# Kernel tuning notes

Hardware: AMD Instinct MI355X
Metric: run time of the kernel (lower is better)

The kernel has to match this reference:

```python
import jax, jax.numpy as jnp
import numpy as np

EMBED_DIM = 1024
NUM_HEADS = 16
HEAD_DIM = EMBED_DIM // NUM_HEADS


def setup_inputs() -> dict:
    key = jax.random.key(0)
    ks = jax.random.split(key, 5)
    B, T, C = 2, 2048, EMBED_DIM
    s_in = 1.0 / np.sqrt(C)
    x = jax.random.normal(ks[0], (B, T, C), dtype=jnp.float32)
    W_qkv = jax.random.normal(ks[1], (C, 3 * C), dtype=jnp.float32) * s_in
    b_qkv = jnp.zeros((3 * C,), dtype=jnp.float32)
    W_out = jax.random.normal(ks[2], (C, C), dtype=jnp.float32) * s_in
    b_out = jnp.zeros((C,), dtype=jnp.float32)
    return {"x": x, "W_qkv": W_qkv, "b_qkv": b_qkv, "W_out": W_out, "b_out": b_out}


def reference(x, W_qkv, b_qkv, W_out, b_out):
    B, T, C = x.shape
    H, D = NUM_HEADS, HEAD_DIM
    qkv = x @ W_qkv + b_qkv                      # [B,T,3C]
    qkv = qkv.reshape(B, T, 3, H, D)
    q = jnp.transpose(qkv[:, :, 0], (0, 2, 1, 3))  # [B,H,T,D]
    k = jnp.transpose(qkv[:, :, 1], (0, 2, 1, 3))
    v = jnp.transpose(qkv[:, :, 2], (0, 2, 1, 3))
    scores = jnp.einsum('bhtd,bhsd->bhts', q, k) / np.sqrt(D).astype(jnp.float32)
    attn = jax.nn.softmax(scores, axis=-1)
    ctx = jnp.einsum('bhts,bhsd->bhtd', attn, v)   # [B,H,T,D]
    ctx = jnp.transpose(ctx, (0, 2, 1, 3)).reshape(B, T, C)
    return ctx @ W_out + b_out
```

## Files before the change

kernel.cpp:

```cpp
#include <hip/hip_runtime.h>
#include <hip/hip_bf16.h>


typedef __attribute__((ext_vector_type(8)))  short short8;
typedef __attribute__((ext_vector_type(4)))  float floatx4;
typedef __attribute__((ext_vector_type(16))) float floatx16;

__device__ inline ushort f2bf(float f) {
    union { __hip_bfloat16 h; ushort u; } c; c.h = __float2bfloat16(f); return c.u;
}

__device__ inline uint cvt_pk_bf16(float a, float b) {
    uint r;
    asm("v_cvt_pk_bf16_f32 %0, %1, %2" : "=v"(r) : "v"(a), "v"(b));
    return r;
}

__device__ inline void gld16(const ushort* g, ushort* l) {
    __builtin_amdgcn_global_load_lds(
        (__attribute__((address_space(1))) void*)(g),
        (__attribute__((address_space(3))) void*)(l), 16, 0, 0);
}

__device__ inline void tile_transpose(const float* __restrict__ src, ushort* __restrict__ dst,
                                      int R, int C, int rt, int ct, int t, ushort* L)
{
    const int row = t >> 2, cc = (t & 3) * 16;
    const float* sp = src + (long)(rt * 64 + row) * C + ct * 64 + cc;
    ushort tmp[16];
    #pragma unroll
    for (int i = 0; i < 4; i++) {
        float4 v = *(const float4*)(sp + i * 4);
        tmp[i*4+0]=f2bf(v.x); tmp[i*4+1]=f2bf(v.y); tmp[i*4+2]=f2bf(v.z); tmp[i*4+3]=f2bf(v.w);
    }
    *(uint4*)&L[row * 72 + cc]     = *(uint4*)&tmp[0];
    *(uint4*)&L[row * 72 + cc + 8] = *(uint4*)&tmp[8];
    __syncthreads();
    const int c = t >> 2, rc = (t & 3) * 16;
    ushort o[16];
    #pragma unroll
    for (int j = 0; j < 16; j++) o[j] = L[(rc + j) * 72 + c];
    ushort* dp = dst + (long)(ct * 64 + c) * R + rt * 64 + rc;
    *(uint4*)dp       = *(uint4*)&o[0];
    *(uint4*)(dp + 8) = *(uint4*)&o[8];
}

__global__ __launch_bounds__(256) void prep_kernel(
    const float* __restrict__ x, const float* __restrict__ Wqkv, const float* __restrict__ Wout,
    ushort* __restrict__ xb, ushort* __restrict__ wqkvT, ushort* __restrict__ woutT)
{
    __shared__ __align__(16) ushort L[64 * 72];
    const int bid = blockIdx.x, t = threadIdx.x;
    if (bid < 2048) {
        long i = ((long)bid * 256 + t) * 8;
        float4 a = *(const float4*)(x + i);
        float4 b = *(const float4*)(x + i + 4);
        ushort tmp[8] = { f2bf(a.x), f2bf(a.y), f2bf(a.z), f2bf(a.w),
                          f2bf(b.x), f2bf(b.y), f2bf(b.z), f2bf(b.w) };
        *(uint4*)(xb + i) = *(uint4*)tmp;
    } else if (bid < 2048 + 768) {
        int idx = bid - 2048;
        tile_transpose(Wqkv, wqkvT, 1024, 3072, idx & 15, idx >> 4, t, L);
    } else {
        int idx = bid - 2048 - 768;
        tile_transpose(Wout, woutT, 1024, 1024, idx & 15, idx >> 4, t, L);
    }
}

#define QSCALE 0.18033688011112042f

__global__ __launch_bounds__(256, 3) void qkv_gemm_kernel(
    const ushort* __restrict__ A, const ushort* __restrict__ Bt,
    const float* __restrict__ bias,
    ushort* __restrict__ qbuf, ushort* __restrict__ kbuf, ushort* __restrict__ vtG)
{
    __shared__ __align__(16) ushort SMEM[16384];

    const int t = threadIdx.x;
    const int w = t >> 6, lane = t & 63;
    const int r = lane & 15, qq = lane >> 4;
    const int wm = w >> 1, wn = w & 1;

    const int id = blockIdx.x;
    const int xcd = id & 7, cidx = id >> 3;
    const int lx = cidx % 12, ly = cidx / 12;
    const int bx = (xcd & 1) * 12 + lx;
    const int by = (xcd >> 1) * 8 + ly;
    const int rowBase = by * 128, colBase = bx * 128;

    const int s_row = lane >> 2, s_k = (lane & 3) * 8;
    const ushort* aS = A  + (long)(rowBase + w * 32 + s_row) * 1024 + s_k;
    const ushort* bS = Bt + (long)(colBase + w * 32 + s_row) * 1024 + s_k;

    floatx4 acc[4][4] = {};

    gld16(aS,             SMEM + w * 1024);
    gld16(aS + 16 * 1024, SMEM + w * 1024 + 512);
    gld16(bS,             SMEM + 4096 + w * 1024);
    gld16(bS + 16 * 1024, SMEM + 4096 + w * 1024 + 512);
    __syncthreads();

    #pragma unroll 2
    for (int k = 0; k < 32; k++) {
        ushort* cur = SMEM + (k & 1) * 8192;
        if (k < 31) {
            ushort* nxt = SMEM + ((k + 1) & 1) * 8192;
            const int ko = (k + 1) * 32;
            gld16(aS + ko,             nxt + w * 1024);
            gld16(aS + ko + 16 * 1024, nxt + w * 1024 + 512);
            gld16(bS + ko,             nxt + 4096 + w * 1024);
            gld16(bS + ko + 16 * 1024, nxt + 4096 + w * 1024 + 512);
        }
        short8 af[4], bf4[4];
        #pragma unroll
        for (int tm = 0; tm < 4; tm++) af[tm]  = *(const short8*)&cur[(wm * 64 + tm * 16 + r) * 32 + qq * 8];
        #pragma unroll
        for (int tn = 0; tn < 4; tn++) bf4[tn] = *(const short8*)&cur[4096 + (wn * 64 + tn * 16 + r) * 32 + qq * 8];
        #pragma unroll
        for (int tm = 0; tm < 4; tm++)
            #pragma unroll
            for (int tn = 0; tn < 4; tn++)
                acc[tm][tn] = __builtin_amdgcn_mfma_f32_16x16x32_bf16(af[tm], bf4[tn], acc[tm][tn], 0, 0, 0);
        __syncthreads();
    }

    if (colBase < 2048) {
        #pragma unroll
        for (int tn = 0; tn < 4; tn++) {
            int col = colBase + wn * 64 + tn * 16 + r;
            float bvv = bias[col];
            #pragma unroll
            for (int tm = 0; tm < 4; tm++) {
                #pragma unroll
                for (int reg = 0; reg < 4; reg++) {
                    int row = rowBase + wm * 64 + tm * 16 + qq * 4 + reg;
                    float val = acc[tm][tn][reg] + bvv;
                    if (colBase < 1024) qbuf[(long)row * 1024 + col]        = f2bf(val * QSCALE);
                    else                kbuf[(long)row * 1024 + col - 1024] = f2bf(val);
                }
            }
        }
    } else {
        ushort* L = SMEM;
        #pragma unroll
        for (int hh = 0; hh < 2; hh++) {
            __syncthreads();
            if (wn == hh) {
                #pragma unroll
                for (int tn = 0; tn < 4; tn++) {
                    int vc = tn * 16 + r;
                    float bvv = bias[colBase + wn * 64 + vc];
                    #pragma unroll
                    for (int tm = 0; tm < 4; tm++) {
                        int row0 = wm * 64 + tm * 16 + qq * 4;
                        ushort q4[4] = { f2bf(acc[tm][tn][0] + bvv), f2bf(acc[tm][tn][1] + bvv),
                                         f2bf(acc[tm][tn][2] + bvv), f2bf(acc[tm][tn][3] + bvv) };
                        *(uint2*)&L[vc * 136 + row0] = *(uint2*)q4;
                    }
                }
            }
            __syncthreads();
            int d = t >> 2, tq = (t & 3) * 32;
            int h_loc = ((colBase - 2048) >> 6) + hh;
            long vtrow = (long)((rowBase >> 11) * 16 + h_loc) * 64 + d;
            ushort* dst = vtG + vtrow * 2048 + (rowBase & 2047) + tq;
            #pragma unroll
            for (int i = 0; i < 4; i++)
                *(uint4*)(dst + 8 * i) = *(uint4*)&L[d * 136 + tq + 8 * i];
        }
    }
}

__global__ __launch_bounds__(256) void out_gemm_kernel(
    const ushort* __restrict__ A, const ushort* __restrict__ Bt,
    const float* __restrict__ bias, float* __restrict__ out)
{
    __shared__ __align__(16) ushort SMEM[12288];

    const int t = threadIdx.x;
    const int w = t >> 6, lane = t & 63;
    const int r = lane & 15, qq = lane >> 4;
    const int wm = w >> 1, wn = w & 1;

    const int id = blockIdx.x;
    const int xcd = id & 7, cidx = id >> 3;
    const int bx = (xcd & 1) * 8 + (cidx & 7);
    const int by = (xcd >> 1) * 8 + (cidx >> 3);
    const int rowBase = by * 128, colBase = bx * 64;

    const int s_row = lane >> 2, s_k = (lane & 3) * 8;
    const ushort* aS = A  + (long)(rowBase + w * 32 + s_row) * 1024 + s_k;
    const ushort* bS = Bt + (long)(colBase + w * 16 + s_row) * 1024 + s_k;

    floatx4 acc[4][2] = {};

    gld16(aS,             SMEM + w * 1024);
    gld16(aS + 16 * 1024, SMEM + w * 1024 + 512);
    gld16(bS,             SMEM + 4096 + w * 512);
    __syncthreads();

    #pragma unroll 2
    for (int k = 0; k < 32; k++) {
        ushort* cur = SMEM + (k & 1) * 6144;
        if (k < 31) {
            ushort* nxt = SMEM + ((k + 1) & 1) * 6144;
            const int ko = (k + 1) * 32;
            gld16(aS + ko,             nxt + w * 1024);
            gld16(aS + ko + 16 * 1024, nxt + w * 1024 + 512);
            gld16(bS + ko,             nxt + 4096 + w * 512);
        }
        short8 af[4], bf2[2];
        #pragma unroll
        for (int tm = 0; tm < 4; tm++) af[tm]  = *(const short8*)&cur[(wm * 64 + tm * 16 + r) * 32 + qq * 8];
        #pragma unroll
        for (int tn = 0; tn < 2; tn++) bf2[tn] = *(const short8*)&cur[4096 + (wn * 32 + tn * 16 + r) * 32 + qq * 8];
        #pragma unroll
        for (int tm = 0; tm < 4; tm++)
            #pragma unroll
            for (int tn = 0; tn < 2; tn++)
                acc[tm][tn] = __builtin_amdgcn_mfma_f32_16x16x32_bf16(af[tm], bf2[tn], acc[tm][tn], 0, 0, 0);
        __syncthreads();
    }

    #pragma unroll
    for (int tn = 0; tn < 2; tn++) {
        int col = colBase + wn * 32 + tn * 16 + r;
        float bvv = bias[col];
        #pragma unroll
        for (int tm = 0; tm < 4; tm++) {
            #pragma unroll
            for (int reg = 0; reg < 4; reg++) {
                int row = rowBase + wm * 64 + tm * 16 + qq * 4 + reg;
                out[(long)row * 1024 + col] = acc[tm][tn][reg] + bvv;
            }
        }
    }
}

__global__ __launch_bounds__(512, 4) void attn_kernel(
    ushort* __restrict__ qbuf, const ushort* __restrict__ kbuf,
    const ushort* __restrict__ vt)
{
    __shared__ __align__(16) ushort SM[2][2][2][64 * 72];

    const int t = threadIdx.x;
    const int w = t >> 6, lane = t & 63;
    const int m32 = lane & 31, hi = lane >> 5;
    const int h2 = w >> 2, wq = w & 3;

    const int id = blockIdx.x;
    const int j = id >> 3;
    const int bh = (id & 7) * 4 + (j >> 4);
    const int qt = j & 15;
    const int b = bh >> 4, h = bh & 15;
    const long qrow = (long)(b * 2048 + qt * 128 + wq * 32 + m32);

    short8 qfrag[4];
    #pragma unroll
    for (int dc = 0; dc < 4; dc++)
        qfrag[dc] = *(const short8*)(qbuf + qrow * 1024 + h * 64 + dc * 16 + hi * 8);

    short8 vones;
    #pragma unroll
    for (int i = 0; i < 8; i++) vones[i] = (short)0x3F80;

    const int ts = t & 255;
    const int srow = ts >> 2, scol = (ts & 3) * 16;
    const ushort* kP = kbuf + (long)(b * 2048 + h2 * 1024 + srow) * 1024 + h * 64 + scol;
    const ushort* vP = vt + (long)(bh * 64 + srow) * 2048 + h2 * 1024 + scol;

    floatx16 o[2] = {};
    floatx16 lacc = {};

    uint4 kr0, kr1, vr0, vr1;

    kr0 = *(const uint4*)kP;  kr1 = *(const uint4*)(kP + 8);
    vr0 = *(const uint4*)vP;  vr1 = *(const uint4*)(vP + 8);
    {
        ushort* Ks = SM[h2][0][0]; ushort* Vs = SM[h2][0][1];
        *(uint4*)&Ks[srow * 72 + scol]     = kr0;
        *(uint4*)&Ks[srow * 72 + scol + 8] = kr1;
        *(uint4*)&Vs[srow * 72 + scol]     = vr0;
        *(uint4*)&Vs[srow * 72 + scol + 8] = vr1;
    }
    kr0 = *(const uint4*)(kP + 64 * 1024); kr1 = *(const uint4*)(kP + 64 * 1024 + 8);
    vr0 = *(const uint4*)(vP + 64);        vr1 = *(const uint4*)(vP + 64 + 8);
    __syncthreads();

    #pragma unroll 2
    for (int tt = 0; tt < 16; tt++) {
        ushort* Ks = SM[h2][tt & 1][0];
        ushort* Vs = SM[h2][tt & 1][1];

        floatx16 s[2] = {};
        __builtin_amdgcn_s_setprio(1);
        #pragma unroll
        for (int c = 0; c < 2; c++) {
            #pragma unroll
            for (int dc = 0; dc < 4; dc++) {
                short8 kf = *(const short8*)&Ks[(c * 32 + m32) * 72 + dc * 16 + hi * 8];
                s[c] = __builtin_amdgcn_mfma_f32_32x32x16_bf16(kf, qfrag[dc], s[c], 0, 0, 0);
            }
        }
        __builtin_amdgcn_s_setprio(0);

        if (tt < 15) {
            ushort* Kn = SM[h2][(tt + 1) & 1][0];
            ushort* Vn = SM[h2][(tt + 1) & 1][1];
            *(uint4*)&Kn[srow * 72 + scol]     = kr0;
            *(uint4*)&Kn[srow * 72 + scol + 8] = kr1;
            *(uint4*)&Vn[srow * 72 + scol]     = vr0;
            *(uint4*)&Vn[srow * 72 + scol + 8] = vr1;
            if (tt < 14) {
                const ushort* kp = kP + (long)(tt + 2) * 64 * 1024;
                const ushort* vp = vP + (tt + 2) * 64;
                kr0 = *(const uint4*)kp; kr1 = *(const uint4*)(kp + 8);
                vr0 = *(const uint4*)vp; vr1 = *(const uint4*)(vp + 8);
            }
        }

        uint pk[2][8];
        #pragma unroll
        for (int c = 0; c < 2; c++) {
            #pragma unroll
            for (int i = 0; i < 8; i++) {
                float p0 = __builtin_amdgcn_exp2f(s[c][2 * i]);
                float p1 = __builtin_amdgcn_exp2f(s[c][2 * i + 1]);
                pk[c][i] = cvt_pk_bf16(p0, p1);
            }
        }

        __builtin_amdgcn_s_setprio(1);
        #pragma unroll
        for (int c = 0; c < 2; c++) {
            #pragma unroll
            for (int kc = 0; kc < 2; kc++) {
                uint a0 = pk[c][4 * kc + 0], b0 = pk[c][4 * kc + 2];
                asm("v_permlane32_swap_b32 %0, %1" : "+v"(a0), "+v"(b0));
                uint a1 = pk[c][4 * kc + 1], b1 = pk[c][4 * kc + 3];
                asm("v_permlane32_swap_b32 %0, %1" : "+v"(a1), "+v"(b1));
                union { uint u[4]; short8 s8; } cv;
                cv.u[0] = a0; cv.u[1] = a1; cv.u[2] = b0; cv.u[3] = b1;
                #pragma unroll
                for (int dt = 0; dt < 2; dt++) {
                    short8 vf = *(const short8*)&Vs[(dt * 32 + m32) * 72 + c * 32 + kc * 16 + hi * 8];
                    o[dt] = __builtin_amdgcn_mfma_f32_32x32x16_bf16(vf, cv.s8, o[dt], 0, 0, 0);
                }
                lacc = __builtin_amdgcn_mfma_f32_32x32x16_bf16(vones, cv.s8, lacc, 0, 0, 0);
            }
        }
        __builtin_amdgcn_s_setprio(0);

        __syncthreads();
    }

    float* OL = (float*)SM;
    float* LL = OL + 4 * 2048;
    if (h2 == 1) {
        #pragma unroll
        for (int dt = 0; dt < 2; dt++)
            #pragma unroll
            for (int i = 0; i < 16; i++)
                OL[wq * 2048 + (dt * 16 + i) * 64 + lane] = o[dt][i];
        LL[wq * 64 + lane] = lacc[0];
    }
    __syncthreads();
    if (h2 == 0) {
        float inv = 1.f / (lacc[0] + LL[wq * 64 + lane]);
        #pragma unroll
        for (int dt = 0; dt < 2; dt++) {
            #pragma unroll
            for (int i = 0; i < 16; i++) o[dt][i] += OL[wq * 2048 + (dt * 16 + i) * 64 + lane];
            #pragma unroll
            for (int g = 0; g < 4; g++) {
                ushort tmp[4] = { f2bf(o[dt][4*g+0] * inv), f2bf(o[dt][4*g+1] * inv),
                                  f2bf(o[dt][4*g+2] * inv), f2bf(o[dt][4*g+3] * inv) };
                *(uint2*)(qbuf + qrow * 1024 + h * 64 + dt * 32 + g * 8 + hi * 4) = *(uint2*)tmp;
            }
        }
    }
}

extern "C" void kernel_launch(void* const* d_in, const int* in_sizes, int n_in,
                              void* d_out, int out_size, void* d_ws, size_t ws_size,
                              hipStream_t stream) {
    const float* x     = (const float*)d_in[0];
    const float* W_qkv = (const float*)d_in[1];
    const float* b_qkv = (const float*)d_in[2];
    const float* W_out = (const float*)d_in[3];
    const float* b_out = (const float*)d_in[4];
    float* out = (float*)d_out;

    ushort* qbuf  = (ushort*)d_ws;
    ushort* kbuf  = qbuf + (size_t)4096 * 1024;
    ushort* vt    = kbuf + (size_t)4096 * 1024;
    ushort* woutT = vt + (size_t)2048 * 2048;
    ushort* wqkvT = woutT + (size_t)1024 * 1024;

    ushort* xb    = (ushort*)d_out;

    dim3 blk(256);
    prep_kernel<<<3072, blk, 0, stream>>>(x, W_qkv, W_out, xb, wqkvT, woutT);
    qkv_gemm_kernel<<<768, blk, 0, stream>>>(xb, wqkvT, b_qkv, qbuf, kbuf, vt);
    attn_kernel<<<512, dim3(512), 0, stream>>>(qbuf, kbuf, vt);
    out_gemm_kernel<<<512, blk, 0, stream>>>(qbuf, woutT, b_out, out);
}
```

Baseline: 187.2 us.

## Drop KV split in attention; each block handles 256 queries over full KV

Before, each block had two wave groups that each covered half the key/value sequence for 128 queries, and their partial outputs were merged through shared memory. Now all 8 waves work on 256 different query rows, sharing one K/V tile stream over the whole sequence, and the grid is halved. This removes the cross-group merge and doubles K/V tile reuse per block. The costs are a serial loop twice as long per block, only 256 blocks (about one per CU), and a lower launch-bounds occupancy hint, which may leave less latency hiding.

```diff
diff --git a/kernel.cpp b/kernel.cpp
--- a/kernel.cpp
+++ b/kernel.cpp
@@ -237,23 +237,22 @@
     }
 }
 
-__global__ __launch_bounds__(512, 4) void attn_kernel(
+__global__ __launch_bounds__(512, 2) void attn_kernel(
     ushort* __restrict__ qbuf, const ushort* __restrict__ kbuf,
     const ushort* __restrict__ vt)
 {
-    __shared__ __align__(16) ushort SM[2][2][2][64 * 72];
+    __shared__ __align__(16) ushort SM[2][2][64 * 72];
 
     const int t = threadIdx.x;
     const int w = t >> 6, lane = t & 63;
     const int m32 = lane & 31, hi = lane >> 5;
-    const int h2 = w >> 2, wq = w & 3;
 
     const int id = blockIdx.x;
     const int j = id >> 3;
-    const int bh = (id & 7) * 4 + (j >> 4);
-    const int qt = j & 15;
+    const int bh = (id & 7) * 4 + (j >> 3);
+    const int qt = j & 7;
     const int b = bh >> 4, h = bh & 15;
-    const long qrow = (long)(b * 2048 + qt * 128 + wq * 32 + m32);
+    const long qrow = (long)(b * 2048 + qt * 256 + w * 32 + m32);
 
     short8 qfrag[4];
     #pragma unroll
@@ -264,33 +263,27 @@
     #pragma unroll
     for (int i = 0; i < 8; i++) vones[i] = (short)0x3F80;
 
-    const int ts = t & 255;
-    const int srow = ts >> 2, scol = (ts & 3) * 16;
-    const ushort* kP = kbuf + (long)(b * 2048 + h2 * 1024 + srow) * 1024 + h * 64 + scol;
-    const ushort* vP = vt + (long)(bh * 64 + srow) * 2048 + h2 * 1024 + scol;
+    const int srow = t >> 3, scol = (t & 7) * 8;
+    const ushort* kP = kbuf + (long)(b * 2048 + srow) * 1024 + h * 64 + scol;
+    const ushort* vP = vt + (long)(bh * 64 + srow) * 2048 + scol;
 
     floatx16 o[2] = {};
     floatx16 lacc = {};
 
-    uint4 kr0, kr1, vr0, vr1;
-
-    kr0 = *(const uint4*)kP;  kr1 = *(const uint4*)(kP + 8);
-    vr0 = *(const uint4*)vP;  vr1 = *(const uint4*)(vP + 8);
-    {
-        ushort* Ks = SM[h2][0][0]; ushort* Vs = SM[h2][0][1];
-        *(uint4*)&Ks[srow * 72 + scol]     = kr0;
-        *(uint4*)&Ks[srow * 72 + scol + 8] = kr1;
-        *(uint4*)&Vs[srow * 72 + scol]     = vr0;
-        *(uint4*)&Vs[srow * 72 + scol + 8] = vr1;
-    }
-    kr0 = *(const uint4*)(kP + 64 * 1024); kr1 = *(const uint4*)(kP + 64 * 1024 + 8);
-    vr0 = *(const uint4*)(vP + 64);        vr1 = *(const uint4*)(vP + 64 + 8);
+    uint4 kr0, vr0;
+
+    kr0 = *(const uint4*)kP;
+    vr0 = *(const uint4*)vP;
+    *(uint4*)&SM[0][0][srow * 72 + scol] = kr0;
+    *(uint4*)&SM[0][1][srow * 72 + scol] = vr0;
+    kr0 = *(const uint4*)(kP + 64 * 1024);
+    vr0 = *(const uint4*)(vP + 64);
     __syncthreads();
 
     #pragma unroll 2
-    for (int tt = 0; tt < 16; tt++) {
-        ushort* Ks = SM[h2][tt & 1][0];
-        ushort* Vs = SM[h2][tt & 1][1];
+    for (int tt = 0; tt < 32; tt++) {
+        ushort* Ks = SM[tt & 1][0];
+        ushort* Vs = SM[tt & 1][1];
 
         floatx16 s[2] = {};
         __builtin_amdgcn_s_setprio(1);
@@ -304,18 +297,12 @@
         }
         __builtin_amdgcn_s_setprio(0);
 
-        if (tt < 15) {
-            ushort* Kn = SM[h2][(tt + 1) & 1][0];
-            ushort* Vn = SM[h2][(tt + 1) & 1][1];
-            *(uint4*)&Kn[srow * 72 + scol]     = kr0;
-            *(uint4*)&Kn[srow * 72 + scol + 8] = kr1;
-            *(uint4*)&Vn[srow * 72 + scol]     = vr0;
-            *(uint4*)&Vn[srow * 72 + scol + 8] = vr1;
-            if (tt < 14) {
-                const ushort* kp = kP + (long)(tt + 2) * 64 * 1024;
-                const ushort* vp = vP + (tt + 2) * 64;
-                kr0 = *(const uint4*)kp; kr1 = *(const uint4*)(kp + 8);
-                vr0 = *(const uint4*)vp; vr1 = *(const uint4*)(vp + 8);
+        if (tt < 31) {
+            *(uint4*)&SM[(tt + 1) & 1][0][srow * 72 + scol] = kr0;
+            *(uint4*)&SM[(tt + 1) & 1][1][srow * 72 + scol] = vr0;
+            if (tt < 30) {
+                kr0 = *(const uint4*)(kP + (long)(tt + 2) * 64 * 1024);
+                vr0 = *(const uint4*)(vP + (tt + 2) * 64);
             }
         }
 
@@ -354,29 +341,15 @@
         __syncthreads();
     }
 
-    float* OL = (float*)SM;
-    float* LL = OL + 4 * 2048;
-    if (h2 == 1) {
-        #pragma unroll
-        for (int dt = 0; dt < 2; dt++)
-            #pragma unroll
-            for (int i = 0; i < 16; i++)
-                OL[wq * 2048 + (dt * 16 + i) * 64 + lane] = o[dt][i];
-        LL[wq * 64 + lane] = lacc[0];
-    }
-    __syncthreads();
-    if (h2 == 0) {
-        float inv = 1.f / (lacc[0] + LL[wq * 64 + lane]);
-        #pragma unroll
-        for (int dt = 0; dt < 2; dt++) {
-            #pragma unroll
-            for (int i = 0; i < 16; i++) o[dt][i] += OL[wq * 2048 + (dt * 16 + i) * 64 + lane];
-            #pragma unroll
-            for (int g = 0; g < 4; g++) {
-                ushort tmp[4] = { f2bf(o[dt][4*g+0] * inv), f2bf(o[dt][4*g+1] * inv),
-                                  f2bf(o[dt][4*g+2] * inv), f2bf(o[dt][4*g+3] * inv) };
-                *(uint2*)(qbuf + qrow * 1024 + h * 64 + dt * 32 + g * 8 + hi * 4) = *(uint2*)tmp;
-            }
+    float inv = 1.f / lacc[0];
+
+    #pragma unroll
+    for (int dt = 0; dt < 2; dt++) {
+        #pragma unroll
+        for (int g = 0; g < 4; g++) {
+            ushort tmp[4] = { f2bf(o[dt][4*g+0] * inv), f2bf(o[dt][4*g+1] * inv),
+                              f2bf(o[dt][4*g+2] * inv), f2bf(o[dt][4*g+3] * inv) };
+            *(uint2*)(qbuf + qrow * 1024 + h * 64 + dt * 32 + g * 8 + hi * 4) = *(uint2*)tmp;
         }
     }
 }
@@ -402,6 +375,6 @@
     dim3 blk(256);
     prep_kernel<<<3072, blk, 0, stream>>>(x, W_qkv, W_out, xb, wqkvT, woutT);
     qkv_gemm_kernel<<<768, blk, 0, stream>>>(xb, wqkvT, b_qkv, qbuf, kbuf, vt);
-    attn_kernel<<<512, dim3(512), 0, stream>>>(qbuf, kbuf, vt);
+    attn_kernel<<<256, dim3(512), 0, stream>>>(qbuf, kbuf, vt);
     out_gemm_kernel<<<512, blk, 0, stream>>>(qbuf, woutT, b_out, out);
 }
```

Result: faster. 178.9 us (median of 2 runs) (-4.5%).
